# Optimization experiments

Measured on AMD Instinct MI355X. Metric: run time of the kernel, lower is better.

## Reference

```python
import jax, jax.numpy as jnp
import numpy as np

B, S, H, K, V = 1024, 50, 128, 4, 100000
ROUTING_TIMES = 3

def _squash(c):
    # c: [B,K,1,H]
    cap_norm = jnp.sum(jnp.square(c), -1, keepdims=True)
    scalar_factor = cap_norm / (1.0 + cap_norm) / jnp.sqrt(cap_norm + 1e-9)
    return scalar_factor * c

def setup_inputs() -> dict:
    key = jax.random.key(0)
    k1, k2, k3, k4, k5, k6 = jax.random.split(key, 6)
    item_seq = jax.random.randint(k1, (B, S), 0, V)
    mask = jax.random.randint(k2, (B, S), 0, 2).astype(jnp.float32)
    item = jax.random.randint(k3, (B, 1), 0, V)
    emb = jax.random.normal(k4, (V, H), dtype=jnp.float32) * 0.02
    W = jax.random.normal(k5, (H, H), dtype=jnp.float32) * (1.0 / np.sqrt(H))
    # bilinear_type==0 -> capsule routing logits initialized with randn
    capsule_weight0 = jax.random.normal(k6, (B, K, S), dtype=jnp.float32)
    return {"item_seq": item_seq, "mask": mask, "item": item,
            "emb": emb, "W": W, "capsule_weight0": capsule_weight0}

def reference(item_seq, mask, item, emb, W, capsule_weight0):
    # padding_idx=0: lookups see a zeroed row 0 (and get no grad there),
    # but calculate_loss uses the raw weight matrix.
    emb_lookup = emb.at[0].set(0.0)
    seq_emb = emb_lookup[item_seq]          # [B,S,H]
    item_e = emb_lookup[item[:, 0]]         # [B,H]  (squeeze(1))

    # CapsuleNetwork, bilinear_type==0: Linear(H,H,no bias) then repeat_interleave along hidden
    h = seq_emb @ W.T                        # [B,S,H]
    hat = jnp.repeat(h, K, axis=2)           # [B,S,H*K] (repeat_interleave semantics)
    hat = hat.reshape(B, S, K, H).transpose(0, 2, 1, 3)  # [B,K,S,H]
    hat_iter = jax.lax.stop_gradient(hat)    # stop_grad=True (detach)

    atten_mask = jnp.broadcast_to(mask[:, None, :], (B, K, S))
    cw = capsule_weight0
    cap = None
    for i in range(ROUTING_TIMES):
        # torch F.softmax with no dim on a 3-D tensor uses dim=0 (batch axis) -- faithful
        sw = jax.nn.softmax(cw, axis=0)
        sw = jnp.where(atten_mask == 0, 0.0, sw)[:, :, None, :]  # [B,K,1,S]
        src = hat_iter if i < ROUTING_TIMES - 1 else hat
        cap = _squash(sw @ src)                                   # [B,K,1,H]
        if i < ROUTING_TIMES - 1:
            delta = (hat_iter @ jnp.swapaxes(cap, 3, 2)).reshape(B, K, S)
            cw = cw + delta

    user_emb = cap.reshape(B, K, H)          # multi_interest_emb

    # hard readout: pick interest with max dot against target item
    cos = jnp.einsum('bkh,bh->bk', user_emb, item_e)
    k_index = jnp.argmax(cos, axis=1)        # [B]
    best = jnp.take_along_axis(user_emb, k_index[:, None, None], axis=1)[:, 0]  # [B,H]

    # cross-entropy over all items (raw embedding weight)
    scores = best @ emb.T                    # [B,V]
    logp = jax.nn.log_softmax(scores, axis=-1)
    loss = -jnp.mean(jnp.take_along_axis(logp, item, axis=1))
    return user_emb, loss
```

## Files before the change

kernel.cpp:

```cpp
#include <hip/hip_runtime.h>
#include <math.h>

#define BB 1024
#define SS 50
#define SSP 51
#define HH 128
#define KK 4
#define VV 100000
#define NVT 782
#define NVT8 784
#define VPAD (NVT8*128)
#define KS (KK*SS)
#define NHM 400
#define NPAD_LAST 96.0f

typedef __attribute__((ext_vector_type(8))) short bf16x8;
typedef __attribute__((ext_vector_type(4))) float f32x4;

__device__ __forceinline__ ushort f2bf(float x) {
  unsigned u = __float_as_uint(x);
  unsigned r = u + 0x7FFF + ((u >> 16) & 1);
  return (ushort)(r >> 16);
}
__device__ __forceinline__ float bf2f(ushort u) {
  return __uint_as_float(((unsigned)u) << 16);
}
__device__ __forceinline__ bf16x8 cvt8(float4 a, float4 b) {
  bf16x8 r;
  r[0] = (short)f2bf(a.x); r[1] = (short)f2bf(a.y);
  r[2] = (short)f2bf(a.z); r[3] = (short)f2bf(a.w);
  r[4] = (short)f2bf(b.x); r[5] = (short)f2bf(b.y);
  r[6] = (short)f2bf(b.z); r[7] = (short)f2bf(b.w);
  return r;
}

__global__ __launch_bounds__(256) void k_conv(const float* __restrict__ emb,
                                              ushort* __restrict__ embb) {
  size_t i = ((size_t)blockIdx.x * 256 + threadIdx.x) * 4;
  ushort4 o;
  if (i < (size_t)VV * HH) {
    float4 v = *(const float4*)&emb[i];
    o = make_ushort4(f2bf(v.x), f2bf(v.y), f2bf(v.z), f2bf(v.w));
  } else {
    o = make_ushort4(0, 0, 0, 0);
  }
  *(ushort4*)&embb[i] = o;
}

__global__ __launch_bounds__(256) void k_pre(const float* __restrict__ emb,
                                             const float* __restrict__ cw0,
                                             float* __restrict__ cm,
                                             float* __restrict__ s1,
                                             float* __restrict__ s2,
                                             float* __restrict__ accum,
                                             const int* __restrict__ item_seq,
                                             const float* __restrict__ W,
                                             ushort* __restrict__ hb16) {
  const int t = threadIdx.x;
  if (blockIdx.x < NHM) {
    __shared__ __align__(16) ushort sWf[32 * 512];
    const int w = t >> 6;
    const int lane = t & 63;
    const int lr = lane & 15;
    const int lq = lane >> 4;
    const int m0 = blockIdx.x * 128;

#pragma unroll
    for (int it = 0; it < 8; ++it) {
      int pos = t + it * 256;
      int ch = pos >> 6, l = pos & 63;
      int n = (ch & 7) * 16 + (l & 15);
      int k0 = (ch >> 3) * 32 + (l >> 4) * 8;
      float4 a = *(const float4*)&W[n * HH + k0];
      float4 b = *(const float4*)&W[n * HH + k0 + 4];
      *(bf16x8*)&sWf[ch * 512 + l * 8] = cvt8(a, b);
    }

    bf16x8 af[4][2];
#pragma unroll
    for (int vv = 0; vv < 2; ++vv) {
      int m = m0 + w * 32 + vv * 16 + lr;
      int idx = item_seq[m];
#pragma unroll
      for (int ks = 0; ks < 4; ++ks) {
        if (idx != 0) {
          float4 a = *(const float4*)&emb[(size_t)idx * HH + ks * 32 + lq * 8];
          float4 b = *(const float4*)&emb[(size_t)idx * HH + ks * 32 + lq * 8 + 4];
          af[ks][vv] = cvt8(a, b);
        } else {
          af[ks][vv] = (bf16x8){0, 0, 0, 0, 0, 0, 0, 0};
        }
      }
    }
    __syncthreads();

    f32x4 acc[8][2];
#pragma unroll
    for (int nt = 0; nt < 8; ++nt)
#pragma unroll
      for (int vv = 0; vv < 2; ++vv) acc[nt][vv] = (f32x4){0.f, 0.f, 0.f, 0.f};

#pragma unroll
    for (int ks = 0; ks < 4; ++ks) {
      bf16x8 bw[8];
#pragma unroll
      for (int nt = 0; nt < 8; ++nt)
        bw[nt] = *(const bf16x8*)&sWf[(ks * 8 + nt) * 512 + lane * 8];
#pragma unroll
      for (int nt = 0; nt < 8; ++nt)
#pragma unroll
        for (int vv = 0; vv < 2; ++vv)
          acc[nt][vv] = __builtin_amdgcn_mfma_f32_16x16x32_bf16(af[ks][vv], bw[nt], acc[nt][vv], 0, 0, 0);
    }

#pragma unroll
    for (int nt = 0; nt < 8; ++nt)
#pragma unroll
      for (int vv = 0; vv < 2; ++vv)
#pragma unroll
        for (int r = 0; r < 4; ++r) {
          int m = m0 + w * 32 + vv * 16 + lq * 4 + r;
          hb16[(size_t)m * HH + nt * 16 + lr] = f2bf(acc[nt][vv][r]);
        }
  } else {
    __shared__ float red[256];
    const int c = blockIdx.x - NHM;
    if (t < 8) s1[t * KS + c] = 0.f;
    if (t >= 8 && t < 16) s2[(t - 8) * KS + c] = 0.f;
    if (c < 4) accum[c * 256 + t] = 0.f;
    float s = 0.f;
    for (int b = t; b < BB; b += 256) s += __expf(cw0[(size_t)b * KS + c]);
    red[t] = s;
    __syncthreads();
    for (int o = 128; o > 0; o >>= 1) {
      if (t < o) red[t] += red[t + o];
      __syncthreads();
    }
    if (t == 0) cm[c] = red[0];
  }
}

__global__ __launch_bounds__(256) void k_route(const float* __restrict__ cwsrc,
                                               float* __restrict__ cwdst,
                                               const ushort* __restrict__ hb16,
                                               const float* __restrict__ csum,
                                               int nslots,
                                               const float* __restrict__ mask,
                                               int last,
                                               float* __restrict__ out_ue,
                                               const float* __restrict__ emb,
                                               const int* __restrict__ item,
                                               ushort* __restrict__ bestb,
                                               float* __restrict__ csnext,
                                               float* __restrict__ si) {
  __shared__ ushort shT[128 * SSP];
  __shared__ float swl[KS];
  __shared__ float c32p[256];
  __shared__ float c32[128];
  __shared__ float csq[128];
  __shared__ float ie4r[32];
  __shared__ float ie4z[32];
  __shared__ float fac[4];
  __shared__ float cosk[4];
  __shared__ float cosr[4];
  __shared__ int kb;
  const int t = threadIdx.x;
  const int b = blockIdx.x;

  for (int p = t; p < (SS * HH) / 4; p += 256) {
    int flat = 4 * p;
    int s = flat >> 7, col = flat & 127;
    ushort4 v = *(const ushort4*)&hb16[(size_t)b * SS * HH + flat];
    shT[(col + 0) * SSP + s] = v.x;
    shT[(col + 1) * SSP + s] = v.y;
    shT[(col + 2) * SSP + s] = v.z;
    shT[(col + 3) * SSP + s] = v.w;
  }
  if (t < KS) {
    float den = 0.f;
    for (int g2 = 0; g2 < nslots; ++g2) den += csum[g2 * KS + t];
    float v = __expf(cwsrc[(size_t)b * KS + t]) / den;
    if (mask[b * SS + (t % SS)] == 0.0f) v = 0.0f;
    swl[t] = v;
  }
  __syncthreads();

  {
    int col = t & 127;
    int half = t >> 7;
    int k = col >> 5;
    float acc = 0.f;
    const float* swk = &swl[k * SS + half * 25];
    const ushort* hc = &shT[col * SSP + half * 25];
    for (int s = 0; s < 25; ++s) acc += swk[s] * bf2f(hc[s]);
    c32p[t] = acc;
  }
  __syncthreads();
  if (t < 128) c32[t] = c32p[t] + c32p[t + 128];
  __syncthreads();
  if (t < 4) {
    float nrm = 0.f;
#pragma unroll
    for (int j = 0; j < 32; ++j) { float c = c32[32 * t + j]; nrm += c * c; }
    nrm *= 4.0f;
    fac[t] = nrm / (1.0f + nrm) / sqrtf(nrm + 1e-9f);
  }
  __syncthreads();
  if (t < 128) csq[t] = c32[t] * fac[t >> 5];
  __syncthreads();

  if (!last) {
    if (t < KS) {
      int k = t / SS, s = t % SS;
      const float* cq = &csq[32 * k];
      float d = 0.f;
#pragma unroll
      for (int j = 0; j < 32; ++j) d += bf2f(shT[(32 * k + j) * SSP + s]) * cq[j];
      float nv = cwsrc[(size_t)b * KS + t] + 4.0f * d;
      cwdst[(size_t)b * KS + t] = nv;
      atomicAdd(&csnext[(b & 7) * KS + t], __expf(nv));
    }
  } else {
    for (int hh = t; hh < 512; hh += 256) {
      int k = hh >> 7, r = (hh & 127) >> 2;
      out_ue[(size_t)b * 512 + hh] = csq[32 * k + r];
    }
    if (t < 32) {
      int idx = item[b];
      const float* e = emb + (size_t)idx * HH + 4 * t;
      float v = e[0] + e[1] + e[2] + e[3];
      ie4r[t] = v;
      ie4z[t] = (idx == 0) ? 0.f : v;
    }
    __syncthreads();
    if (t < 4) {
      float cz = 0.f, cr = 0.f;
#pragma unroll
      for (int j = 0; j < 32; ++j) {
        cz += csq[32 * t + j] * ie4z[j];
        cr += csq[32 * t + j] * ie4r[j];
      }
      cosk[t] = cz; cosr[t] = cr;
    }
    __syncthreads();
    if (t == 0) {
      int kbest = 0; float bv = cosk[0];
#pragma unroll
      for (int k = 1; k < 4; ++k) if (cosk[k] > bv) { bv = cosk[k]; kbest = k; }
      kb = kbest;
      si[b] = cosr[kbest];
    }
    __syncthreads();
    if (t < 128) bestb[(size_t)b * HH + t] = f2bf(csq[32 * kb + (t >> 2)]);
  }
}

__global__ __launch_bounds__(256) void k_score_mfma(const ushort* __restrict__ bestb,
                                                    const ushort* __restrict__ embb,
                                                    float* __restrict__ accum) {
  const int lin = blockIdx.x;
  const int xcd = lin & 7;
  const int g = lin >> 3;
  const int bt8 = g & 7;
  const int vt = xcd * (NVT8 / 8) + (g >> 3);
  if (vt >= NVT) return;

  __shared__ __align__(16) ushort sB[32 * 512];
  __shared__ float ssm[128][4];
  const int t = threadIdx.x;
  const int w = t >> 6;
  const int lane = t & 63;
  const int lr = lane & 15;
  const int lq = lane >> 4;
  const int b0 = bt8 * 128;
  const int v0 = vt * 128 + w * 32;

  bf16x8 af[4][2];
#pragma unroll
  for (int ks = 0; ks < 4; ++ks)
#pragma unroll
    for (int vv = 0; vv < 2; ++vv)
      af[ks][vv] = *(const bf16x8*)&embb[(size_t)(v0 + vv * 16 + lr) * HH + ks * 32 + lq * 8];

#pragma unroll
  for (int it = 0; it < 8; ++it) {
    int pos = t + it * 256;
    int ch = pos >> 6;
    int l = pos & 63;
    int ks = ch >> 3, bt = ch & 7;
    *(bf16x8*)&sB[ch * 512 + l * 8] =
        *(const bf16x8*)&bestb[(size_t)(b0 + bt * 16 + (l & 15)) * HH + ks * 32 + (l >> 4) * 8];
  }

  f32x4 acc[8][2];
#pragma unroll
  for (int bt = 0; bt < 8; ++bt)
#pragma unroll
    for (int vv = 0; vv < 2; ++vv) acc[bt][vv] = (f32x4){0.f, 0.f, 0.f, 0.f};

  __syncthreads();

  bf16x8 bcur[8];
#pragma unroll
  for (int bt = 0; bt < 8; ++bt)
    bcur[bt] = *(const bf16x8*)&sB[bt * 512 + lane * 8];

#pragma unroll
  for (int ks = 0; ks < 4; ++ks) {
    bf16x8 bnxt[8];
    if (ks < 3) {
#pragma unroll
      for (int bt = 0; bt < 8; ++bt)
        bnxt[bt] = *(const bf16x8*)&sB[((ks + 1) * 8 + bt) * 512 + lane * 8];
    }
#pragma unroll
    for (int bt = 0; bt < 8; ++bt)
#pragma unroll
      for (int vv = 0; vv < 2; ++vv)
        acc[bt][vv] = __builtin_amdgcn_mfma_f32_16x16x32_bf16(af[ks][vv], bcur[bt], acc[bt][vv], 0, 0, 0);
    if (ks < 3) {
#pragma unroll
      for (int bt = 0; bt < 8; ++bt) bcur[bt] = bnxt[bt];
    }
  }

#pragma unroll
  for (int bt = 0; bt < 8; ++bt) {
    float s = 0.f;
#pragma unroll
    for (int vv = 0; vv < 2; ++vv)
#pragma unroll
      for (int r = 0; r < 4; ++r) s += __expf(acc[bt][vv][r]);
    s += __shfl_xor(s, 16);
    s += __shfl_xor(s, 32);
    if (lq == 0) ssm[bt * 16 + lr][w] = s;
  }
  __syncthreads();
  if (t < 128) {
    float s = ssm[t][0] + ssm[t][1] + ssm[t][2] + ssm[t][3];
    atomicAdd(&accum[b0 + t], s);
  }
}

__global__ __launch_bounds__(256) void k_loss(const float* __restrict__ accum,
                                              const float* __restrict__ si,
                                              float* __restrict__ outloss) {
  __shared__ float red[256];
  const int t = threadIdx.x;
  float s = 0.f;
  for (int b = t; b < BB; b += 256)
    s += logf(accum[b] - NPAD_LAST) - si[b];
  red[t] = s;
  __syncthreads();
  for (int o = 128; o > 0; o >>= 1) {
    if (t < o) red[t] += red[t + o];
    __syncthreads();
  }
  if (t == 0) outloss[0] = red[0] / (float)BB;
}

extern "C" void kernel_launch(void* const* d_in, const int* in_sizes, int n_in,
                              void* d_out, int out_size, void* d_ws, size_t ws_size,
                              hipStream_t stream) {
  const int*   item_seq = (const int*)d_in[0];
  const float* mask     = (const float*)d_in[1];
  const int*   item     = (const int*)d_in[2];
  const float* emb      = (const float*)d_in[3];
  const float* W        = (const float*)d_in[4];
  const float* cw0      = (const float*)d_in[5];
  float* out = (float*)d_out;
  float* outloss = out + (size_t)BB * KK * HH;

  float* ws = (float*)d_ws;
  float* cm    = ws;
  float* s1    = cm + 256;
  float* s2    = s1 + 8 * KS;
  float* si    = s2 + 8 * KS;
  float* accum = si + BB;
  float* cw    = accum + BB;
  ushort* hb16  = (ushort*)(cw + (size_t)BB * KS);
  ushort* embb  = hb16 + (size_t)BB * SS * HH;
  ushort* bestb = embb + (size_t)VPAD * HH;

  k_pre<<<dim3(NHM + KS), 256, 0, stream>>>(emb, cw0, cm, s1, s2, accum,
                                            item_seq, W, hb16);
  k_conv<<<dim3((VPAD * HH) / 1024), 256, 0, stream>>>(emb, embb);

  k_route<<<dim3(BB), 256, 0, stream>>>(cw0, cw, hb16, cm, 1, mask, 0, out, emb, item, bestb, s1, si);
  k_route<<<dim3(BB), 256, 0, stream>>>(cw, cw, hb16, s1, 8, mask, 0, out, emb, item, bestb, s2, si);
  k_route<<<dim3(BB), 256, 0, stream>>>(cw, cw, hb16, s2, 8, mask, 1, out, emb, item, bestb, s1, si);

  k_score_mfma<<<dim3(NVT8 * 8), 256, 0, stream>>>(bestb, embb, accum);
  k_loss<<<dim3(1), 256, 0, stream>>>(accum, si, outloss);
}
```

Measured before the change: 200.4 us.

## Fuse embedding conversion into pre kernel and restructure score kernel with persistent B tiles

Merges the fp32→bf16 embedding conversion into the k_pre launch as extra grid-stride blocks, removing one kernel launch and letting the conversion overlap the projection GEMM. The score kernel now holds each wave's 64-row bestb tile in registers, loops over 7 vocab tiles per block on a smaller grid, and drops the LDS staging and mid-kernel sync. The target vector is pre-scaled by log2(e) so exp2f replaces __expf. The padding correction constant changes to match the new padded-row count. The larger register footprint may reduce occupancy.

```diff
diff --git a/kernel.cpp b/kernel.cpp
--- a/kernel.cpp
+++ b/kernel.cpp
@@ -12,7 +12,13 @@
 #define VPAD (NVT8*128)
 #define KS (KK*SS)
 #define NHM 400
-#define NPAD_LAST 96.0f
+#define NPAD_ALL 352.0f
+#define CONVB 2048
+#define LOG2E 1.44269504f
+
+#define SVPB 7
+#define SNCH 14
+#define SGRID (8*8*SNCH)
 
 typedef __attribute__((ext_vector_type(8))) short bf16x8;
 typedef __attribute__((ext_vector_type(4))) float f32x4;
@@ -32,19 +38,6 @@
   r[4] = (short)f2bf(b.x); r[5] = (short)f2bf(b.y);
   r[6] = (short)f2bf(b.z); r[7] = (short)f2bf(b.w);
   return r;
-}
-
-__global__ __launch_bounds__(256) void k_conv(const float* __restrict__ emb,
-                                              ushort* __restrict__ embb) {
-  size_t i = ((size_t)blockIdx.x * 256 + threadIdx.x) * 4;
-  ushort4 o;
-  if (i < (size_t)VV * HH) {
-    float4 v = *(const float4*)&emb[i];
-    o = make_ushort4(f2bf(v.x), f2bf(v.y), f2bf(v.z), f2bf(v.w));
-  } else {
-    o = make_ushort4(0, 0, 0, 0);
-  }
-  *(ushort4*)&embb[i] = o;
 }
 
 __global__ __launch_bounds__(256) void k_pre(const float* __restrict__ emb,
@@ -55,7 +48,8 @@
                                              float* __restrict__ accum,
                                              const int* __restrict__ item_seq,
                                              const float* __restrict__ W,
-                                             ushort* __restrict__ hb16) {
+                                             ushort* __restrict__ hb16,
+                                             ushort* __restrict__ embb) {
   const int t = threadIdx.x;
   if (blockIdx.x < NHM) {
     __shared__ __align__(16) ushort sWf[32 * 512];
@@ -122,7 +116,7 @@
           int m = m0 + w * 32 + vv * 16 + lq * 4 + r;
           hb16[(size_t)m * HH + nt * 16 + lr] = f2bf(acc[nt][vv][r]);
         }
-  } else {
+  } else if (blockIdx.x < NHM + KS) {
     __shared__ float red[256];
     const int c = blockIdx.x - NHM;
     if (t < 8) s1[t * KS + c] = 0.f;
@@ -137,6 +131,19 @@
       __syncthreads();
     }
     if (t == 0) cm[c] = red[0];
+  } else {
+    const size_t stride = (size_t)CONVB * 256 * 4;
+    for (size_t i = ((size_t)(blockIdx.x - NHM - KS) * 256 + t) * 4;
+         i < (size_t)VPAD * HH; i += stride) {
+      ushort4 o;
+      if (i < (size_t)VV * HH) {
+        float4 v = *(const float4*)&emb[i];
+        o = make_ushort4(f2bf(v.x), f2bf(v.y), f2bf(v.z), f2bf(v.w));
+      } else {
+        o = make_ushort4(0, 0, 0, 0);
+      }
+      *(ushort4*)&embb[i] = o;
+    }
   }
 }
 
@@ -251,7 +258,7 @@
       si[b] = cosr[kbest];
     }
     __syncthreads();
-    if (t < 128) bestb[(size_t)b * HH + t] = f2bf(csq[32 * kb + (t >> 2)]);
+    if (t < 128) bestb[(size_t)b * HH + t] = f2bf(csq[32 * kb + (t >> 2)] * LOG2E);
   }
 }
 
@@ -260,86 +267,79 @@
                                                     float* __restrict__ accum) {
   const int lin = blockIdx.x;
   const int xcd = lin & 7;
-  const int g = lin >> 3;
-  const int bt8 = g & 7;
-  const int vt = xcd * (NVT8 / 8) + (g >> 3);
-  if (vt >= NVT) return;
-
-  __shared__ __align__(16) ushort sB[32 * 512];
-  __shared__ float ssm[128][4];
+  const int j = lin >> 3;
+  const int bt8 = j & 7;
+  const int chunk = j >> 3;
+  const int vt0 = xcd * 98 + chunk * SVPB;
+
+  __shared__ float ssm[128][2];
   const int t = threadIdx.x;
   const int w = t >> 6;
   const int lane = t & 63;
   const int lr = lane & 15;
   const int lq = lane >> 4;
-  const int b0 = bt8 * 128;
-  const int v0 = vt * 128 + w * 32;
-
-  bf16x8 af[4][2];
+  const int wv = w >> 1;
+  const int wb = w & 1;
+  const int b0 = bt8 * 128 + wb * 64;
+
+  bf16x8 bf[4][4];
 #pragma unroll
   for (int ks = 0; ks < 4; ++ks)
 #pragma unroll
-    for (int vv = 0; vv < 2; ++vv)
-      af[ks][vv] = *(const bf16x8*)&embb[(size_t)(v0 + vv * 16 + lr) * HH + ks * 32 + lq * 8];
-
-#pragma unroll
-  for (int it = 0; it < 8; ++it) {
-    int pos = t + it * 256;
-    int ch = pos >> 6;
-    int l = pos & 63;
-    int ks = ch >> 3, bt = ch & 7;
-    *(bf16x8*)&sB[ch * 512 + l * 8] =
-        *(const bf16x8*)&bestb[(size_t)(b0 + bt * 16 + (l & 15)) * HH + ks * 32 + (l >> 4) * 8];
-  }
-
-  f32x4 acc[8][2];
-#pragma unroll
-  for (int bt = 0; bt < 8; ++bt)
-#pragma unroll
-    for (int vv = 0; vv < 2; ++vv) acc[bt][vv] = (f32x4){0.f, 0.f, 0.f, 0.f};
-
-  __syncthreads();
-
-  bf16x8 bcur[8];
-#pragma unroll
-  for (int bt = 0; bt < 8; ++bt)
-    bcur[bt] = *(const bf16x8*)&sB[bt * 512 + lane * 8];
-
-#pragma unroll
-  for (int ks = 0; ks < 4; ++ks) {
-    bf16x8 bnxt[8];
-    if (ks < 3) {
-#pragma unroll
-      for (int bt = 0; bt < 8; ++bt)
-        bnxt[bt] = *(const bf16x8*)&sB[((ks + 1) * 8 + bt) * 512 + lane * 8];
-    }
-#pragma unroll
-    for (int bt = 0; bt < 8; ++bt)
-#pragma unroll
-      for (int vv = 0; vv < 2; ++vv)
-        acc[bt][vv] = __builtin_amdgcn_mfma_f32_16x16x32_bf16(af[ks][vv], bcur[bt], acc[bt][vv], 0, 0, 0);
-    if (ks < 3) {
-#pragma unroll
-      for (int bt = 0; bt < 8; ++bt) bcur[bt] = bnxt[bt];
-    }
-  }
-
-#pragma unroll
-  for (int bt = 0; bt < 8; ++bt) {
-    float s = 0.f;
-#pragma unroll
-    for (int vv = 0; vv < 2; ++vv)
-#pragma unroll
-      for (int r = 0; r < 4; ++r) s += __expf(acc[bt][vv][r]);
+    for (int bt = 0; bt < 4; ++bt)
+      bf[ks][bt] = *(const bf16x8*)&bestb[(size_t)(b0 + bt * 16 + lr) * HH + ks * 32 + lq * 8];
+
+  const ushort* pv[4];
+#pragma unroll
+  for (int vv = 0; vv < 4; ++vv)
+    pv[vv] = &embb[(size_t)(vt0 * 128 + wv * 64 + vv * 16 + lr) * HH + lq * 8];
+
+  float sacc[4] = {0.f, 0.f, 0.f, 0.f};
+
+  for (int i = 0; i < SVPB; ++i) {
+    bf16x8 af[4][4];
+#pragma unroll
+    for (int vv = 0; vv < 4; ++vv)
+#pragma unroll
+      for (int ks = 0; ks < 4; ++ks)
+        af[ks][vv] = *(const bf16x8*)&pv[vv][ks * 32];
+
+    f32x4 acc[4][4];
+#pragma unroll
+    for (int bt = 0; bt < 4; ++bt)
+#pragma unroll
+      for (int vv = 0; vv < 4; ++vv) acc[bt][vv] = (f32x4){0.f, 0.f, 0.f, 0.f};
+
+#pragma unroll
+    for (int ks = 0; ks < 4; ++ks)
+#pragma unroll
+      for (int bt = 0; bt < 4; ++bt)
+#pragma unroll
+        for (int vv = 0; vv < 4; ++vv)
+          acc[bt][vv] = __builtin_amdgcn_mfma_f32_16x16x32_bf16(af[ks][vv], bf[ks][bt], acc[bt][vv], 0, 0, 0);
+
+#pragma unroll
+    for (int bt = 0; bt < 4; ++bt) {
+      float s = 0.f;
+#pragma unroll
+      for (int vv = 0; vv < 4; ++vv)
+#pragma unroll
+        for (int r = 0; r < 4; ++r) s += exp2f(acc[bt][vv][r]);
+      sacc[bt] += s;
+    }
+#pragma unroll
+    for (int vv = 0; vv < 4; ++vv) pv[vv] += 128 * HH;
+  }
+
+#pragma unroll
+  for (int bt = 0; bt < 4; ++bt) {
+    float s = sacc[bt];
     s += __shfl_xor(s, 16);
     s += __shfl_xor(s, 32);
-    if (lq == 0) ssm[bt * 16 + lr][w] = s;
-  }
-  __syncthreads();
-  if (t < 128) {
-    float s = ssm[t][0] + ssm[t][1] + ssm[t][2] + ssm[t][3];
-    atomicAdd(&accum[b0 + t], s);
-  }
+    if (lq == 0) ssm[wb * 64 + bt * 16 + lr][wv] = s;
+  }
+  __syncthreads();
+  if (t < 128) atomicAdd(&accum[bt8 * 128 + t], ssm[t][0] + ssm[t][1]);
 }
 
 __global__ __launch_bounds__(256) void k_loss(const float* __restrict__ accum,
@@ -349,7 +349,7 @@
   const int t = threadIdx.x;
   float s = 0.f;
   for (int b = t; b < BB; b += 256)
-    s += logf(accum[b] - NPAD_LAST) - si[b];
+    s += logf(accum[b] - NPAD_ALL) - si[b];
   red[t] = s;
   __syncthreads();
   for (int o = 128; o > 0; o >>= 1) {
@@ -382,14 +382,13 @@
   ushort* embb  = hb16 + (size_t)BB * SS * HH;
   ushort* bestb = embb + (size_t)VPAD * HH;
 
-  k_pre<<<dim3(NHM + KS), 256, 0, stream>>>(emb, cw0, cm, s1, s2, accum,
-                                            item_seq, W, hb16);
-  k_conv<<<dim3((VPAD * HH) / 1024), 256, 0, stream>>>(emb, embb);
+  k_pre<<<dim3(NHM + KS + CONVB), 256, 0, stream>>>(emb, cw0, cm, s1, s2, accum,
+                                                    item_seq, W, hb16, embb);
 
   k_route<<<dim3(BB), 256, 0, stream>>>(cw0, cw, hb16, cm, 1, mask, 0, out, emb, item, bestb, s1, si);
   k_route<<<dim3(BB), 256, 0, stream>>>(cw, cw, hb16, s1, 8, mask, 0, out, emb, item, bestb, s2, si);
   k_route<<<dim3(BB), 256, 0, stream>>>(cw, cw, hb16, s2, 8, mask, 1, out, emb, item, bestb, s1, si);
 
-  k_score_mfma<<<dim3(NVT8 * 8), 256, 0, stream>>>(bestb, embb, accum);
+  k_score_mfma<<<dim3(SGRID), 256, 0, stream>>>(bestb, embb, accum);
   k_loss<<<dim3(1), 256, 0, stream>>>(accum, si, outloss);
 }
```

Measured after the change: 216.2 us. 7.9% more time.
